# Performance work log

Hardware: AMD Instinct MI355X
Metric: run time of the kernel (lower is better)

## Reference

```python
import jax, jax.numpy as jnp
import numpy as np

NUM_HEADS = 16
LN_EPS = 1e-5

def _gelu(x):
    return jax.nn.gelu(x, approximate=False)  # torch default GELU is exact (erf)

def setup_inputs() -> dict:
    key = jax.random.key(0)
    ks = jax.random.split(key, 12)
    B, S, E = 2, 2048, 1024
    H = E // 2
    s = lambda fan_in: 1.0 / np.sqrt(fan_in)
    inp = {
        "x": jax.random.normal(ks[0], (B, S, E), jnp.float32),
        "Wq": jax.random.normal(ks[1], (E, E), jnp.float32) * s(E),
        "bq": jnp.zeros((E,), jnp.float32),
        "Wk": jax.random.normal(ks[2], (E, E), jnp.float32) * s(E),
        "bk": jnp.zeros((E,), jnp.float32),
        "Wv": jax.random.normal(ks[3], (E, E), jnp.float32) * s(E),
        "bv": jnp.zeros((E,), jnp.float32),
        "Wo": jax.random.normal(ks[4], (E, E), jnp.float32) * s(E),
        "bo": jnp.zeros((E,), jnp.float32),
        "dp_w1": jax.random.normal(ks[5], (E, H), jnp.float32) * s(E),
        "dp_b1": jnp.zeros((H,), jnp.float32),
        "ln_g": jnp.ones((H,), jnp.float32),
        "ln_b": jnp.zeros((H,), jnp.float32),
        "dp_w2": jax.random.normal(ks[6], (H, 1), jnp.float32) * s(H),
        "dp_b2": jnp.zeros((1,), jnp.float32),
        "g_w1": jax.random.normal(ks[7], (1, 16), jnp.float32),
        "g_b1": jnp.zeros((16,), jnp.float32),
        "g_w2": jax.random.normal(ks[8], (16, 1), jnp.float32) * s(16),
        "g_b2": jnp.zeros((1,), jnp.float32),
    }
    return inp


def reference(x, Wq, bq, Wk, bk, Wv, bv, Wo, bo,
              dp_w1, dp_b1, ln_g, ln_b, dp_w2, dp_b2,
              g_w1, g_b1, g_w2, g_b2):
    B, S, E = x.shape
    Hn = NUM_HEADS
    Dh = E // Hn
    scale = Dh ** -0.5

    Q = (x @ Wq + bq).reshape(B, S, Hn, Dh)
    K = (x @ Wk + bk).reshape(B, S, Hn, Dh)
    V = (x @ Wv + bv).reshape(B, S, Hn, Dh)

    # (B, H, q, k)
    logits = jnp.einsum('bqhd,bkhd->bhqk', Q, K) * scale
    causal = jnp.tril(jnp.ones((S, S), bool))
    logits = jnp.where(causal, logits, -jnp.inf)
    attn = jax.nn.softmax(logits, axis=-1)

    # drift probe: Linear -> LayerNorm -> GELU -> Linear, squeeze -> (B, S)
    h = x @ dp_w1 + dp_b1
    mu = h.mean(-1, keepdims=True)
    var = ((h - mu) ** 2).mean(-1, keepdims=True)
    h = (h - mu) / jnp.sqrt(var + LN_EPS) * ln_g + ln_b
    drift = (_gelu(h) @ dp_w2 + dp_b2)[..., 0]

    # drift_to_gate: Linear(1,16) -> GELU -> Linear(16,1) -> Tanh -> (B, S)
    g = _gelu(drift[..., None] * g_w1[0] + g_b1)
    gate = jnp.tanh(g @ g_w2 + g_b2)[..., 0]  # (B, S), indexed by key position

    gated = attn * gate[:, None, None, :]  # dropout p=0 -> identity
    out = jnp.einsum('bhqk,bkhd->bqhd', gated, V).reshape(B, S, E)
    return out @ Wo + bo
```

## Files before the change

kernel.cpp:

```cpp
#include <hip/hip_runtime.h>
#include <math.h>
#include <stdint.h>

#define B_   2
#define S_   2048
#define E_   1024
#define NH   16
#define DH   64
#define HID  512
#define NCAT 3584
#define MTOK 4096

typedef unsigned short ushort_t;
typedef short  s16x8  __attribute__((ext_vector_type(8)));
typedef unsigned short us4 __attribute__((ext_vector_type(4)));
typedef float  f32x4  __attribute__((ext_vector_type(4)));

static constexpr float LN_EPS    = 1e-5f;
static constexpr float SCALE     = 0.125f;
static constexpr float INV_SQRT2 = 0.70710678118654752440f;

__device__ __forceinline__ float gelu_exact(float v) {
    return 0.5f * v * (1.0f + erff(v * INV_SQRT2));
}

__device__ __forceinline__ ushort_t f2bf(float f) {
    unsigned int u = __float_as_uint(f);
    unsigned int r = u + 0x7fffu + ((u >> 16) & 1u);
    return (ushort_t)(r >> 16);
}
__device__ __forceinline__ float bf2f(ushort_t s) {
    return __uint_as_float(((unsigned int)s) << 16);
}

__device__ __forceinline__ void stage16(const void* g, void* ldsbase) {
#if __has_builtin(__builtin_amdgcn_global_load_lds)
    __builtin_amdgcn_global_load_lds(
        (const __attribute__((address_space(1))) void*)g,
        (__attribute__((address_space(3))) void*)ldsbase, 16, 0, 0);
#else
    ((uint4*)ldsbase)[threadIdx.x & 63] = *(const uint4*)g;
#endif
}

__device__ __forceinline__ void xcd_swizzle(int gx, int gy, int& bx, int& by) {
    const int T = gx * gy;
    const int lin = blockIdx.y * gx + blockIdx.x;
    const int work = (lin & 7) * (T >> 3) + (lin >> 3);
    bx = work % gx;
    by = work / gx;
}

__global__ __launch_bounds__(256) void split_kernel(
    const float* __restrict__ src, ushort_t* __restrict__ dh,
    ushort_t* __restrict__ dl, int n4)
{
    int i = blockIdx.x * 256 + threadIdx.x;
    if (i >= n4) return;
    float4 v = ((const float4*)src)[i];
    float vv[4] = {v.x, v.y, v.z, v.w};
    us4 h, l;
    #pragma unroll
    for (int j = 0; j < 4; ++j) {
        ushort_t hh = f2bf(vv[j]);
        h[j] = hh;
        l[j] = f2bf(vv[j] - bf2f(hh));
    }
    *(us4*)&dh[i * 4] = h;
    *(us4*)&dl[i * 4] = l;
}

__global__ __launch_bounds__(256) void transpose_split_kernel(
    const float* __restrict__ W, int N,
    ushort_t* __restrict__ th, ushort_t* __restrict__ tl)
{
    __shared__ float tile[32][33];
    const int k0 = blockIdx.x * 32, n0 = blockIdx.y * 32;
    const int t = threadIdx.x;
    const int r = t >> 3, c4 = (t & 7) * 4;

    float4 v = *(const float4*)&W[(size_t)(k0 + r) * N + n0 + c4];
    tile[r][c4 + 0] = v.x; tile[r][c4 + 1] = v.y;
    tile[r][c4 + 2] = v.z; tile[r][c4 + 3] = v.w;
    __syncthreads();

    us4 h, l;
    #pragma unroll
    for (int i = 0; i < 4; ++i) {
        float x = tile[c4 + i][r];
        ushort_t hh = f2bf(x);
        h[i] = hh;
        l[i] = f2bf(x - bf2f(hh));
    }
    *(us4*)&th[(size_t)(n0 + r) * E_ + k0 + c4] = h;
    *(us4*)&tl[(size_t)(n0 + r) * E_ + k0 + c4] = l;
}

__global__ void concat_bias_kernel(
    const float* __restrict__ bq, const float* __restrict__ bk,
    const float* __restrict__ bv, const float* __restrict__ b1,
    float* __restrict__ bcat)
{
    int i = blockIdx.x * 256 + threadIdx.x;
    if (i >= NCAT) return;
    float v;
    if      (i < 1024) v = bq[i];
    else if (i < 2048) v = bk[i - 1024];
    else if (i < 3072) v = bv[i - 2048];
    else               v = b1[i - 3072];
    bcat[i] = v;
}

struct GemmCtx {
    int lane, w, wr, wc;
};

__device__ __forceinline__ void gemm_core(
    const ushort_t* __restrict__ Ah, const ushort_t* __restrict__ Al,
    const ushort_t* __restrict__ Bh, const ushort_t* __restrict__ Bl,
    int row0, int col0, int Kd,
    ushort_t* Ahs, ushort_t* Als, ushort_t* Bhs, ushort_t* Bls,
    f32x4 (&acc)[4][4], const GemmCtx& cx)
{
    const int lr = cx.lane >> 2;
    const int lc = (cx.lane & 3) * 8;

    for (int k0 = 0; k0 < Kd; k0 += 32) {
        #pragma unroll
        for (int ii = 0; ii < 2; ++ii) {
            const int r0 = (cx.w * 2 + ii) * 16;
            const size_t ga = (size_t)(row0 + r0 + lr) * Kd + k0 + lc;
            const size_t gb = (size_t)(col0 + r0 + lr) * Kd + k0 + lc;
            stage16(Ah + ga, &Ahs[r0 * 32]);
            stage16(Al + ga, &Als[r0 * 32]);
            stage16(Bh + gb, &Bhs[r0 * 32]);
            stage16(Bl + gb, &Bls[r0 * 32]);
        }
        __syncthreads();

        const int rA = cx.wr * 64 + (cx.lane & 15);
        const int rB = cx.wc * 64 + (cx.lane & 15);
        const int kq = (cx.lane >> 4) * 8;
        s16x8 fah[4], fal[4], fbh[4], fbl[4];
        #pragma unroll
        for (int i = 0; i < 4; ++i) {
            fah[i] = *(const s16x8*)&Ahs[(rA + i * 16) * 32 + kq];
            fal[i] = *(const s16x8*)&Als[(rA + i * 16) * 32 + kq];
            fbh[i] = *(const s16x8*)&Bhs[(rB + i * 16) * 32 + kq];
            fbl[i] = *(const s16x8*)&Bls[(rB + i * 16) * 32 + kq];
        }
        __builtin_amdgcn_s_setprio(1);
        #pragma unroll
        for (int i = 0; i < 4; ++i)
            #pragma unroll
            for (int j = 0; j < 4; ++j) {
                acc[i][j] = __builtin_amdgcn_mfma_f32_16x16x32_bf16(fah[i], fbh[j], acc[i][j], 0, 0, 0);
                acc[i][j] = __builtin_amdgcn_mfma_f32_16x16x32_bf16(fah[i], fbl[j], acc[i][j], 0, 0, 0);
                acc[i][j] = __builtin_amdgcn_mfma_f32_16x16x32_bf16(fal[i], fbh[j], acc[i][j], 0, 0, 0);
            }
        __builtin_amdgcn_s_setprio(0);
        __syncthreads();
    }
}

__global__ __launch_bounds__(256) void mfma_gemm_qkvh_kernel(
    const ushort_t* __restrict__ Ah, const ushort_t* __restrict__ Al,
    const ushort_t* __restrict__ Bh, const ushort_t* __restrict__ Bl,
    const float* __restrict__ bias,
    ushort_t* __restrict__ Qh, ushort_t* __restrict__ Ql,
    ushort_t* __restrict__ Kh, ushort_t* __restrict__ Kl,
    float* __restrict__ v32, float* __restrict__ h32)
{
    __shared__ __align__(16) ushort_t Ahs[128 * 32];
    __shared__ __align__(16) ushort_t Als[128 * 32];
    __shared__ __align__(16) ushort_t Bhs[128 * 32];
    __shared__ __align__(16) ushort_t Bls[128 * 32];

    int bx, by;
    xcd_swizzle(28, 32, bx, by);
    const int row0 = by * 128, col0 = bx * 128;

    GemmCtx cx;
    cx.lane = threadIdx.x & 63;
    cx.w    = threadIdx.x >> 6;
    cx.wr   = cx.w >> 1; cx.wc = cx.w & 1;

    f32x4 acc[4][4] = {};
    gemm_core(Ah, Al, Bh, Bl, row0, col0, E_, Ahs, Als, Bhs, Bls, acc, cx);

    const int crow = row0 + cx.wr * 64 + ((cx.lane >> 4) * 4);
    const int ccol0 = col0 + cx.wc * 64 + (cx.lane & 15);

    #pragma unroll
    for (int j = 0; j < 4; ++j) {
        const int gcol = ccol0 + j * 16;
        const float bv = bias[gcol];
        #pragma unroll
        for (int i = 0; i < 4; ++i)
            #pragma unroll
            for (int r = 0; r < 4; ++r) {
                const int row = crow + i * 16 + r;
                float val = acc[i][j][r] + bv;
                if (gcol < 1024) {
                    val *= SCALE;
                    ushort_t hi = f2bf(val);
                    Qh[(size_t)row * 1024 + gcol] = hi;
                    Ql[(size_t)row * 1024 + gcol] = f2bf(val - bf2f(hi));
                } else if (gcol < 2048) {
                    ushort_t hi = f2bf(val);
                    Kh[(size_t)row * 1024 + gcol - 1024] = hi;
                    Kl[(size_t)row * 1024 + gcol - 1024] = f2bf(val - bf2f(hi));
                } else if (gcol < 3072) {
                    v32[(size_t)row * 1024 + gcol - 2048] = val;
                } else {
                    h32[(size_t)row * 512 + gcol - 3072] = val;
                }
            }
    }
}

__global__ __launch_bounds__(256) void mfma_gemm_kernel(
    const ushort_t* __restrict__ Ah, const ushort_t* __restrict__ Al,
    const ushort_t* __restrict__ Bh, const ushort_t* __restrict__ Bl,
    const float* __restrict__ bias,
    float* __restrict__ C, int N, int Kd)
{
    __shared__ __align__(16) ushort_t Ahs[128 * 32];
    __shared__ __align__(16) ushort_t Als[128 * 32];
    __shared__ __align__(16) ushort_t Bhs[128 * 32];
    __shared__ __align__(16) ushort_t Bls[128 * 32];

    int bx, by;
    xcd_swizzle(gridDim.x, gridDim.y, bx, by);
    const int row0 = by * 128, col0 = bx * 128;

    GemmCtx cx;
    cx.lane = threadIdx.x & 63;
    cx.w    = threadIdx.x >> 6;
    cx.wr   = cx.w >> 1; cx.wc = cx.w & 1;

    f32x4 acc[4][4] = {};
    gemm_core(Ah, Al, Bh, Bl, row0, col0, Kd, Ahs, Als, Bhs, Bls, acc, cx);

    const int crow = row0 + cx.wr * 64 + ((cx.lane >> 4) * 4);
    const int ccol = col0 + cx.wc * 64 + (cx.lane & 15);
    #pragma unroll
    for (int j = 0; j < 4; ++j) {
        const float bv = bias[ccol + j * 16];
        #pragma unroll
        for (int i = 0; i < 4; ++i)
            #pragma unroll
            for (int r = 0; r < 4; ++r)
                C[(size_t)(crow + i * 16 + r) * N + ccol + j * 16] = acc[i][j][r] + bv;
    }
}

__global__ __launch_bounds__(256) void ln_gate_kernel(
    const float* __restrict__ h32,
    const float* __restrict__ lng, const float* __restrict__ lnb,
    const float* __restrict__ w2,  const float* __restrict__ b2,
    const float* __restrict__ gw1, const float* __restrict__ gb1,
    const float* __restrict__ gw2, const float* __restrict__ gb2,
    float* __restrict__ gate)
{
    const int row  = blockIdx.x * 4 + (threadIdx.x >> 6);
    const int lane = threadIdx.x & 63;
    const float* h = h32 + (size_t)row * 512;

    float4 a = *(const float4*)&h[lane * 4];
    float4 b = *(const float4*)&h[256 + lane * 4];
    float va[8] = {a.x, a.y, a.z, a.w, b.x, b.y, b.z, b.w};

    float sum = 0.f, sq = 0.f;
    #pragma unroll
    for (int j = 0; j < 8; ++j) { sum += va[j]; sq += va[j] * va[j]; }
    #pragma unroll
    for (int o = 1; o < 64; o <<= 1) {
        sum += __shfl_xor(sum, o);
        sq  += __shfl_xor(sq,  o);
    }
    const float mu  = sum * (1.f / HID);
    const float inv = 1.f / sqrtf(sq * (1.f / HID) - mu * mu + LN_EPS);

    float4 g0 = *(const float4*)&lng[lane * 4];
    float4 g1 = *(const float4*)&lng[256 + lane * 4];
    float4 o0 = *(const float4*)&lnb[lane * 4];
    float4 o1 = *(const float4*)&lnb[256 + lane * 4];
    float4 w0 = *(const float4*)&w2[lane * 4];
    float4 w1 = *(const float4*)&w2[256 + lane * 4];
    float gg[8] = {g0.x, g0.y, g0.z, g0.w, g1.x, g1.y, g1.z, g1.w};
    float bb[8] = {o0.x, o0.y, o0.z, o0.w, o1.x, o1.y, o1.z, o1.w};
    float ww[8] = {w0.x, w0.y, w0.z, w0.w, w1.x, w1.y, w1.z, w1.w};

    float part = 0.f;
    #pragma unroll
    for (int j = 0; j < 8; ++j) {
        float nx = (va[j] - mu) * inv * gg[j] + bb[j];
        part += gelu_exact(nx) * ww[j];
    }
    #pragma unroll
    for (int o = 1; o < 64; o <<= 1) part += __shfl_xor(part, o);

    if (lane == 0) {
        float drift = part + b2[0];
        float gacc = gb2[0];
        #pragma unroll
        for (int i = 0; i < 16; ++i) {
            float t = fmaf(drift, gw1[i], gb1[i]);
            gacc = fmaf(gelu_exact(t), gw2[i], gacc);
        }
        gate[row] = tanhf(gacc);
    }
}

__global__ __launch_bounds__(256) void v_transpose_kernel(
    const float* __restrict__ v32, const float* __restrict__ gate,
    ushort_t* __restrict__ Vth, ushort_t* __restrict__ Vtl)
{
    __shared__ float T[64 * 68];
    const int kt = blockIdx.x, bh = blockIdx.y;
    const int b = bh >> 4, h = bh & 15;
    const int tid = threadIdx.x;

    #pragma unroll
    for (int it = 0; it < 4; ++it) {
        int idx = tid + it * 256;
        int tokr = idx >> 4, f4 = idx & 15;
        int tok = b * S_ + kt * 64 + tokr;
        float g = gate[tok];
        float4 v = *(const float4*)&v32[(size_t)tok * 1024 + h * 64 + f4 * 4];
        T[(f4 * 4 + 0) * 68 + tokr] = v.x * g;
        T[(f4 * 4 + 1) * 68 + tokr] = v.y * g;
        T[(f4 * 4 + 2) * 68 + tokr] = v.z * g;
        T[(f4 * 4 + 3) * 68 + tokr] = v.w * g;
    }
    __syncthreads();

    const int d = tid >> 2, t0 = (tid & 3) * 16;
    const size_t obase = (size_t)bh * 64 * S_ + (size_t)d * S_ + kt * 64 + t0;
    s16x8 h8[2], l8[2];
    #pragma unroll
    for (int u = 0; u < 16; ++u) {
        float f = T[d * 68 + t0 + u];
        ushort_t hh = f2bf(f);
        h8[u >> 3][u & 7] = (short)hh;
        l8[u >> 3][u & 7] = (short)f2bf(f - bf2f(hh));
    }
    *(s16x8*)&Vth[obase]     = h8[0];
    *(s16x8*)&Vth[obase + 8] = h8[1];
    *(s16x8*)&Vtl[obase]     = l8[0];
    *(s16x8*)&Vtl[obase + 8] = l8[1];
}

__global__ __launch_bounds__(256) void attn_mfma_kernel(
    const ushort_t* __restrict__ Qh, const ushort_t* __restrict__ Ql,
    const ushort_t* __restrict__ Kh, const ushort_t* __restrict__ Kl,
    const ushort_t* __restrict__ Vth, const ushort_t* __restrict__ Vtl,
    ushort_t* __restrict__ ch, ushort_t* __restrict__ cl)
{
    __shared__ __align__(16) ushort_t Qhs[64 * 72], Qls[64 * 72];
    __shared__ __align__(16) ushort_t Khs[64 * 72], Kls[64 * 72];
    __shared__ __align__(16) ushort_t Vhs[64 * 72], Vls[64 * 72];
    __shared__ __align__(16) unsigned int Ps[4 * 16 * 68];

    const int tid  = threadIdx.x;
    const int lane = tid & 63;
    const int w    = tid >> 6;
    const int g    = lane >> 4;
    const int c    = lane & 15;

    const int lin  = blockIdx.y * 32 + blockIdx.x;
    const int work = (lin & 7) * 128 + (lin >> 3);
    const int bh   = work >> 5;
    const int qt   = 31 - (work & 31);
    const int b    = bh >> 4, h = bh & 15;
    const int q0   = qt * 64;

    const size_t qkb = (size_t)b * S_ * 1024 + h * 64;
    const size_t vtb = (size_t)bh * 64 * S_;

    #pragma unroll
    for (int it = 0; it < 2; ++it) {
        int c2 = tid + it * 256;
        int row = c2 >> 3, sl = c2 & 7;
        s16x8 vh = *(const s16x8*)&Qh[qkb + (size_t)(q0 + row) * 1024 + sl * 8];
        s16x8 vl = *(const s16x8*)&Ql[qkb + (size_t)(q0 + row) * 1024 + sl * 8];
        *(s16x8*)&Qhs[row * 72 + sl * 8] = vh;
        *(s16x8*)&Qls[row * 72 + sl * 8] = vl;
    }

    f32x4 o4[4] = {};
    float m[4], l[4];
    #pragma unroll
    for (int r = 0; r < 4; ++r) { m[r] = -INFINITY; l[r] = 0.f; }

    const int pbase = w * (16 * 68);
    __syncthreads();

    s16x8 qfh[2], qfl[2];
    #pragma unroll
    for (int ks = 0; ks < 2; ++ks) {
        qfh[ks] = *(const s16x8*)&Qhs[(w * 16 + c) * 72 + ks * 32 + g * 8];
        qfl[ks] = *(const s16x8*)&Qls[(w * 16 + c) * 72 + ks * 32 + g * 8];
    }

    const int srow = tid >> 3, ssl = tid & 7;
    const int srow1 = (tid + 256) >> 3, ssl1 = (tid + 256) & 7;

    s16x8 pkh[2], pkl[2], pvh[2], pvl[2];
    {
        pkh[0] = *(const s16x8*)&Kh [qkb + (size_t)srow  * 1024 + ssl  * 8];
        pkl[0] = *(const s16x8*)&Kl [qkb + (size_t)srow  * 1024 + ssl  * 8];
        pvh[0] = *(const s16x8*)&Vth[vtb + (size_t)srow  * S_ + ssl  * 8];
        pvl[0] = *(const s16x8*)&Vtl[vtb + (size_t)srow  * S_ + ssl  * 8];
        pkh[1] = *(const s16x8*)&Kh [qkb + (size_t)srow1 * 1024 + ssl1 * 8];
        pkl[1] = *(const s16x8*)&Kl [qkb + (size_t)srow1 * 1024 + ssl1 * 8];
        pvh[1] = *(const s16x8*)&Vth[vtb + (size_t)srow1 * S_ + ssl1 * 8];
        pvl[1] = *(const s16x8*)&Vtl[vtb + (size_t)srow1 * S_ + ssl1 * 8];
    }

    for (int kt = 0; kt <= qt; ++kt) {
        const int k0 = kt * 64;
        *(s16x8*)&Khs[srow  * 72 + ssl  * 8] = pkh[0];
        *(s16x8*)&Kls[srow  * 72 + ssl  * 8] = pkl[0];
        *(s16x8*)&Vhs[srow  * 72 + ssl  * 8] = pvh[0];
        *(s16x8*)&Vls[srow  * 72 + ssl  * 8] = pvl[0];
        *(s16x8*)&Khs[srow1 * 72 + ssl1 * 8] = pkh[1];
        *(s16x8*)&Kls[srow1 * 72 + ssl1 * 8] = pkl[1];
        *(s16x8*)&Vhs[srow1 * 72 + ssl1 * 8] = pvh[1];
        *(s16x8*)&Vls[srow1 * 72 + ssl1 * 8] = pvl[1];
        __syncthreads();

        if (kt < qt) {
            const int kn = k0 + 64;
            pkh[0] = *(const s16x8*)&Kh [qkb + (size_t)(kn + srow)  * 1024 + ssl  * 8];
            pkl[0] = *(const s16x8*)&Kl [qkb + (size_t)(kn + srow)  * 1024 + ssl  * 8];
            pvh[0] = *(const s16x8*)&Vth[vtb + (size_t)srow  * S_ + kn + ssl  * 8];
            pvl[0] = *(const s16x8*)&Vtl[vtb + (size_t)srow  * S_ + kn + ssl  * 8];
            pkh[1] = *(const s16x8*)&Kh [qkb + (size_t)(kn + srow1) * 1024 + ssl1 * 8];
            pkl[1] = *(const s16x8*)&Kl [qkb + (size_t)(kn + srow1) * 1024 + ssl1 * 8];
            pvh[1] = *(const s16x8*)&Vth[vtb + (size_t)srow1 * S_ + kn + ssl1 * 8];
            pvl[1] = *(const s16x8*)&Vtl[vtb + (size_t)srow1 * S_ + kn + ssl1 * 8];
        }

        f32x4 s4[4] = {};
        __builtin_amdgcn_s_setprio(1);
        #pragma unroll
        for (int j = 0; j < 4; ++j)
            #pragma unroll
            for (int ks = 0; ks < 2; ++ks) {
                s16x8 kfh = *(const s16x8*)&Khs[(c + j * 16) * 72 + ks * 32 + g * 8];
                s16x8 kfl = *(const s16x8*)&Kls[(c + j * 16) * 72 + ks * 32 + g * 8];
                s4[j] = __builtin_amdgcn_mfma_f32_16x16x32_bf16(qfh[ks], kfh, s4[j], 0, 0, 0);
                s4[j] = __builtin_amdgcn_mfma_f32_16x16x32_bf16(qfh[ks], kfl, s4[j], 0, 0, 0);
                s4[j] = __builtin_amdgcn_mfma_f32_16x16x32_bf16(qfl[ks], kfh, s4[j], 0, 0, 0);
            }
        __builtin_amdgcn_s_setprio(0);

        if (kt == qt) {
            #pragma unroll
            for (int j = 0; j < 4; ++j)
                #pragma unroll
                for (int r = 0; r < 4; ++r)
                    if (k0 + c + j * 16 > q0 + w * 16 + g * 4 + r)
                        s4[j][r] = -INFINITY;
        }

        #pragma unroll
        for (int r = 0; r < 4; ++r) {
            float mx = fmaxf(fmaxf(s4[0][r], s4[1][r]), fmaxf(s4[2][r], s4[3][r]));
            #pragma unroll
            for (int o = 1; o < 16; o <<= 1) mx = fmaxf(mx, __shfl_xor(mx, o));
            float mn = fmaxf(m[r], mx);
            float corr = (m[r] == -INFINITY) ? 0.f : __expf(m[r] - mn);
            float ps = 0.f;
            #pragma unroll
            for (int j = 0; j < 4; ++j) {
                float p = __expf(s4[j][r] - mn);
                s4[j][r] = p;
                ps += p;
            }
            #pragma unroll
            for (int o = 1; o < 16; o <<= 1) ps += __shfl_xor(ps, o);
            l[r] = l[r] * corr + ps;
            m[r] = mn;
            #pragma unroll
            for (int j = 0; j < 4; ++j) o4[j][r] *= corr;
        }

        #pragma unroll
        for (int j = 0; j < 4; ++j)
            #pragma unroll
            for (int r = 0; r < 4; ++r) {
                float p = s4[j][r];
                ushort_t hi = f2bf(p);
                ushort_t lo = f2bf(p - bf2f(hi));
                Ps[pbase + (g * 4 + r) * 68 + c + j * 16] =
                    (unsigned int)hi | ((unsigned int)lo << 16);
            }
        asm volatile("s_waitcnt lgkmcnt(0)" ::: "memory");
        __builtin_amdgcn_sched_barrier(0);

        s16x8 pah[2], pal[2];
        #pragma unroll
        for (int ks = 0; ks < 2; ++ks) {
            uint4 a = *(const uint4*)&Ps[pbase + c * 68 + ks * 32 + g * 8];
            uint4 bq = *(const uint4*)&Ps[pbase + c * 68 + ks * 32 + g * 8 + 4];
            unsigned int wd[8] = {a.x, a.y, a.z, a.w, bq.x, bq.y, bq.z, bq.w};
            union { unsigned int u[4]; s16x8 v; } uh, ul;
            #pragma unroll
            for (int t = 0; t < 4; ++t) {
                uh.u[t] = (wd[2 * t] & 0xffffu) | (wd[2 * t + 1] << 16);
                ul.u[t] = (wd[2 * t] >> 16) | (wd[2 * t + 1] & 0xffff0000u);
            }
            pah[ks] = uh.v;
            pal[ks] = ul.v;
        }

        __builtin_amdgcn_s_setprio(1);
        #pragma unroll
        for (int j = 0; j < 4; ++j)
            #pragma unroll
            for (int ks = 0; ks < 2; ++ks) {
                s16x8 vfh = *(const s16x8*)&Vhs[(c + j * 16) * 72 + ks * 32 + g * 8];
                s16x8 vfl = *(const s16x8*)&Vls[(c + j * 16) * 72 + ks * 32 + g * 8];
                o4[j] = __builtin_amdgcn_mfma_f32_16x16x32_bf16(pah[ks], vfh, o4[j], 0, 0, 0);
                o4[j] = __builtin_amdgcn_mfma_f32_16x16x32_bf16(pah[ks], vfl, o4[j], 0, 0, 0);
                o4[j] = __builtin_amdgcn_mfma_f32_16x16x32_bf16(pal[ks], vfh, o4[j], 0, 0, 0);
            }
        __builtin_amdgcn_s_setprio(0);
        __syncthreads();
    }

    float inv[4];
    #pragma unroll
    for (int r = 0; r < 4; ++r) inv[r] = 1.f / l[r];
    #pragma unroll
    for (int j = 0; j < 4; ++j)
        #pragma unroll
        for (int r = 0; r < 4; ++r) {
            float val = o4[j][r] * inv[r];
            int tok = b * S_ + q0 + w * 16 + g * 4 + r;
            int col = h * 64 + c + j * 16;
            ushort_t hi = f2bf(val);
            ch[(size_t)tok * 1024 + col] = hi;
            cl[(size_t)tok * 1024 + col] = f2bf(val - bf2f(hi));
        }
}

extern "C" void kernel_launch(void* const* d_in, const int* in_sizes, int n_in,
                              void* d_out, int out_size, void* d_ws, size_t ws_size,
                              hipStream_t stream)
{
    const float* x    = (const float*)d_in[0];
    const float* Wq   = (const float*)d_in[1];  const float* bq   = (const float*)d_in[2];
    const float* Wk   = (const float*)d_in[3];  const float* bk   = (const float*)d_in[4];
    const float* Wv   = (const float*)d_in[5];  const float* bv   = (const float*)d_in[6];
    const float* Wo   = (const float*)d_in[7];  const float* bo   = (const float*)d_in[8];
    const float* dpw1 = (const float*)d_in[9];  const float* dpb1 = (const float*)d_in[10];
    const float* lng  = (const float*)d_in[11]; const float* lnb  = (const float*)d_in[12];
    const float* dpw2 = (const float*)d_in[13]; const float* dpb2 = (const float*)d_in[14];
    const float* gw1  = (const float*)d_in[15]; const float* gb1  = (const float*)d_in[16];
    const float* gw2  = (const float*)d_in[17]; const float* gb2  = (const float*)d_in[18];
    float* out = (float*)d_out;

    float* ws   = (float*)d_ws;
    float* v32  = ws;
    float* h32  = v32 + (size_t)MTOK * E_;
    float* bcat = h32 + (size_t)MTOK * HID;
    float* gate = bcat + NCAT;
    ushort_t* bp   = (ushort_t*)(gate + MTOK);
    ushort_t* xh   = bp;
    ushort_t* xl   = xh  + (size_t)MTOK * E_;
    ushort_t* bth  = xl  + (size_t)MTOK * E_;
    ushort_t* btl  = bth + (size_t)NCAT * E_;
    ushort_t* woth = btl + (size_t)NCAT * E_;
    ushort_t* wotl = woth + (size_t)E_ * E_;
    ushort_t* Qhb  = wotl + (size_t)E_ * E_;
    ushort_t* Qlb  = Qhb + (size_t)MTOK * E_;
    ushort_t* Khb  = Qlb + (size_t)MTOK * E_;
    ushort_t* Klb  = Khb + (size_t)MTOK * E_;
    ushort_t* Vthb = Klb + (size_t)MTOK * E_;
    ushort_t* Vtlb = Vthb + (size_t)MTOK * E_;
    ushort_t* chb  = xh;
    ushort_t* clb  = xl;

    hipLaunchKernelGGL(split_kernel, dim3(4096), dim3(256), 0, stream,
                       x, xh, xl, MTOK * E_ / 4);
    hipLaunchKernelGGL(transpose_split_kernel, dim3(32, 32), dim3(256), 0, stream,
                       Wq, E_, bth, btl);
    hipLaunchKernelGGL(transpose_split_kernel, dim3(32, 32), dim3(256), 0, stream,
                       Wk, E_, bth + (size_t)1024 * E_, btl + (size_t)1024 * E_);
    hipLaunchKernelGGL(transpose_split_kernel, dim3(32, 32), dim3(256), 0, stream,
                       Wv, E_, bth + (size_t)2048 * E_, btl + (size_t)2048 * E_);
    hipLaunchKernelGGL(transpose_split_kernel, dim3(32, 16), dim3(256), 0, stream,
                       dpw1, HID, bth + (size_t)3072 * E_, btl + (size_t)3072 * E_);
    hipLaunchKernelGGL(transpose_split_kernel, dim3(32, 32), dim3(256), 0, stream,
                       Wo, E_, woth, wotl);
    hipLaunchKernelGGL(concat_bias_kernel, dim3(14), dim3(256), 0, stream,
                       bq, bk, bv, dpb1, bcat);

    hipLaunchKernelGGL(mfma_gemm_qkvh_kernel, dim3(28, 32), dim3(256), 0, stream,
                       xh, xl, bth, btl, bcat, Qhb, Qlb, Khb, Klb, v32, h32);

    hipLaunchKernelGGL(ln_gate_kernel, dim3(MTOK / 4), dim3(256), 0, stream,
                       h32, lng, lnb, dpw2, dpb2, gw1, gb1, gw2, gb2, gate);
    hipLaunchKernelGGL(v_transpose_kernel, dim3(32, 32), dim3(256), 0, stream,
                       v32, gate, Vthb, Vtlb);

    hipLaunchKernelGGL(attn_mfma_kernel, dim3(S_ / 64, B_ * NH), dim3(256), 0, stream,
                       Qhb, Qlb, Khb, Klb, Vthb, Vtlb, chb, clb);

    hipLaunchKernelGGL(mfma_gemm_kernel, dim3(E_ / 128, MTOK / 128), dim3(256), 0, stream,
                       chb, clb, woth, wotl, bo, out, E_, E_);
}
```

Baseline: 440.3 us.

## Widen attention query tile to 128 rows with 8 waves sharing K/V tiles

The attention kernel now processes 128 query rows per block with 512 threads (8 waves), so each staged 64-key K/V tile feeds twice as many query rows and global K/V traffic per query is halved. Shared memory is packed into one buffer, with the P scratch area aliasing the Q staging area, which is dead once Q fragments are in registers. Waves whose 16 rows lie entirely before a key tile skip that tile's MFMA and softmax work. The costs are fewer blocks in the grid, larger causal imbalance inside a block, and a tighter register budget from the launch bounds.

```diff
diff --git a/kernel.cpp b/kernel.cpp
--- a/kernel.cpp
+++ b/kernel.cpp
@@ -352,16 +352,20 @@
     *(s16x8*)&Vtl[obase + 8] = l8[1];
 }
 
-__global__ __launch_bounds__(256) void attn_mfma_kernel(
+__global__ __launch_bounds__(512, 4) void attn_mfma_kernel(
     const ushort_t* __restrict__ Qh, const ushort_t* __restrict__ Ql,
     const ushort_t* __restrict__ Kh, const ushort_t* __restrict__ Kl,
     const ushort_t* __restrict__ Vth, const ushort_t* __restrict__ Vtl,
     ushort_t* __restrict__ ch, ushort_t* __restrict__ cl)
 {
-    __shared__ __align__(16) ushort_t Qhs[64 * 72], Qls[64 * 72];
-    __shared__ __align__(16) ushort_t Khs[64 * 72], Kls[64 * 72];
-    __shared__ __align__(16) ushort_t Vhs[64 * 72], Vls[64 * 72];
-    __shared__ __align__(16) unsigned int Ps[4 * 16 * 68];
+    __shared__ __align__(16) ushort_t smem[36864];
+    ushort_t* const Qhs = smem;
+    ushort_t* const Qls = smem + 9216;
+    ushort_t* const Khs = smem + 18432;
+    ushort_t* const Kls = smem + 23040;
+    ushort_t* const Vhs = smem + 27648;
+    ushort_t* const Vls = smem + 32256;
+    unsigned int* const Ps = (unsigned int*)smem;
 
     const int tid  = threadIdx.x;
     const int lane = tid & 63;
@@ -369,19 +373,19 @@
     const int g    = lane >> 4;
     const int c    = lane & 15;
 
-    const int lin  = blockIdx.y * 32 + blockIdx.x;
-    const int work = (lin & 7) * 128 + (lin >> 3);
-    const int bh   = work >> 5;
-    const int qt   = 31 - (work & 31);
+    const int lin  = blockIdx.y * 16 + blockIdx.x;
+    const int work = (lin & 7) * 64 + (lin >> 3);
+    const int bh   = work >> 4;
+    const int qt   = 15 - (work & 15);
     const int b    = bh >> 4, h = bh & 15;
-    const int q0   = qt * 64;
+    const int q0   = qt * 128;
 
     const size_t qkb = (size_t)b * S_ * 1024 + h * 64;
     const size_t vtb = (size_t)bh * 64 * S_;
 
     #pragma unroll
     for (int it = 0; it < 2; ++it) {
-        int c2 = tid + it * 256;
+        int c2 = tid + it * 512;
         int row = c2 >> 3, sl = c2 & 7;
         s16x8 vh = *(const s16x8*)&Qh[qkb + (size_t)(q0 + row) * 1024 + sl * 8];
         s16x8 vl = *(const s16x8*)&Ql[qkb + (size_t)(q0 + row) * 1024 + sl * 8];
@@ -405,130 +409,120 @@
     }
 
     const int srow = tid >> 3, ssl = tid & 7;
-    const int srow1 = (tid + 256) >> 3, ssl1 = (tid + 256) & 7;
-
-    s16x8 pkh[2], pkl[2], pvh[2], pvl[2];
-    {
-        pkh[0] = *(const s16x8*)&Kh [qkb + (size_t)srow  * 1024 + ssl  * 8];
-        pkl[0] = *(const s16x8*)&Kl [qkb + (size_t)srow  * 1024 + ssl  * 8];
-        pvh[0] = *(const s16x8*)&Vth[vtb + (size_t)srow  * S_ + ssl  * 8];
-        pvl[0] = *(const s16x8*)&Vtl[vtb + (size_t)srow  * S_ + ssl  * 8];
-        pkh[1] = *(const s16x8*)&Kh [qkb + (size_t)srow1 * 1024 + ssl1 * 8];
-        pkl[1] = *(const s16x8*)&Kl [qkb + (size_t)srow1 * 1024 + ssl1 * 8];
-        pvh[1] = *(const s16x8*)&Vth[vtb + (size_t)srow1 * S_ + ssl1 * 8];
-        pvl[1] = *(const s16x8*)&Vtl[vtb + (size_t)srow1 * S_ + ssl1 * 8];
-    }
-
-    for (int kt = 0; kt <= qt; ++kt) {
+
+    s16x8 pkh, pkl, pvh, pvl;
+    pkh = *(const s16x8*)&Kh [qkb + (size_t)srow * 1024 + ssl * 8];
+    pkl = *(const s16x8*)&Kl [qkb + (size_t)srow * 1024 + ssl * 8];
+    pvh = *(const s16x8*)&Vth[vtb + (size_t)srow * S_ + ssl * 8];
+    pvl = *(const s16x8*)&Vtl[vtb + (size_t)srow * S_ + ssl * 8];
+
+    const int ktmax = 2 * qt + 1;
+    const int qwave = q0 + w * 16;
+
+    for (int kt = 0; kt <= ktmax; ++kt) {
         const int k0 = kt * 64;
-        *(s16x8*)&Khs[srow  * 72 + ssl  * 8] = pkh[0];
-        *(s16x8*)&Kls[srow  * 72 + ssl  * 8] = pkl[0];
-        *(s16x8*)&Vhs[srow  * 72 + ssl  * 8] = pvh[0];
-        *(s16x8*)&Vls[srow  * 72 + ssl  * 8] = pvl[0];
-        *(s16x8*)&Khs[srow1 * 72 + ssl1 * 8] = pkh[1];
-        *(s16x8*)&Kls[srow1 * 72 + ssl1 * 8] = pkl[1];
-        *(s16x8*)&Vhs[srow1 * 72 + ssl1 * 8] = pvh[1];
-        *(s16x8*)&Vls[srow1 * 72 + ssl1 * 8] = pvl[1];
+        *(s16x8*)&Khs[srow * 72 + ssl * 8] = pkh;
+        *(s16x8*)&Kls[srow * 72 + ssl * 8] = pkl;
+        *(s16x8*)&Vhs[srow * 72 + ssl * 8] = pvh;
+        *(s16x8*)&Vls[srow * 72 + ssl * 8] = pvl;
         __syncthreads();
 
-        if (kt < qt) {
+        if (kt < ktmax) {
             const int kn = k0 + 64;
-            pkh[0] = *(const s16x8*)&Kh [qkb + (size_t)(kn + srow)  * 1024 + ssl  * 8];
-            pkl[0] = *(const s16x8*)&Kl [qkb + (size_t)(kn + srow)  * 1024 + ssl  * 8];
-            pvh[0] = *(const s16x8*)&Vth[vtb + (size_t)srow  * S_ + kn + ssl  * 8];
-            pvl[0] = *(const s16x8*)&Vtl[vtb + (size_t)srow  * S_ + kn + ssl  * 8];
-            pkh[1] = *(const s16x8*)&Kh [qkb + (size_t)(kn + srow1) * 1024 + ssl1 * 8];
-            pkl[1] = *(const s16x8*)&Kl [qkb + (size_t)(kn + srow1) * 1024 + ssl1 * 8];
-            pvh[1] = *(const s16x8*)&Vth[vtb + (size_t)srow1 * S_ + kn + ssl1 * 8];
-            pvl[1] = *(const s16x8*)&Vtl[vtb + (size_t)srow1 * S_ + kn + ssl1 * 8];
+            pkh = *(const s16x8*)&Kh [qkb + (size_t)(kn + srow) * 1024 + ssl * 8];
+            pkl = *(const s16x8*)&Kl [qkb + (size_t)(kn + srow) * 1024 + ssl * 8];
+            pvh = *(const s16x8*)&Vth[vtb + (size_t)srow * S_ + kn + ssl * 8];
+            pvl = *(const s16x8*)&Vtl[vtb + (size_t)srow * S_ + kn + ssl * 8];
         }
 
-        f32x4 s4[4] = {};
-        __builtin_amdgcn_s_setprio(1);
-        #pragma unroll
-        for (int j = 0; j < 4; ++j)
+        if (k0 <= qwave + 15) {
+            f32x4 s4[4] = {};
+            __builtin_amdgcn_s_setprio(1);
+            #pragma unroll
+            for (int j = 0; j < 4; ++j)
+                #pragma unroll
+                for (int ks = 0; ks < 2; ++ks) {
+                    s16x8 kfh = *(const s16x8*)&Khs[(c + j * 16) * 72 + ks * 32 + g * 8];
+                    s16x8 kfl = *(const s16x8*)&Kls[(c + j * 16) * 72 + ks * 32 + g * 8];
+                    s4[j] = __builtin_amdgcn_mfma_f32_16x16x32_bf16(qfh[ks], kfh, s4[j], 0, 0, 0);
+                    s4[j] = __builtin_amdgcn_mfma_f32_16x16x32_bf16(qfh[ks], kfl, s4[j], 0, 0, 0);
+                    s4[j] = __builtin_amdgcn_mfma_f32_16x16x32_bf16(qfl[ks], kfh, s4[j], 0, 0, 0);
+                }
+            __builtin_amdgcn_s_setprio(0);
+
+            if (k0 + 63 > qwave) {
+                #pragma unroll
+                for (int j = 0; j < 4; ++j)
+                    #pragma unroll
+                    for (int r = 0; r < 4; ++r)
+                        if (k0 + c + j * 16 > qwave + g * 4 + r)
+                            s4[j][r] = -INFINITY;
+            }
+
+            #pragma unroll
+            for (int r = 0; r < 4; ++r) {
+                float mx = fmaxf(fmaxf(s4[0][r], s4[1][r]), fmaxf(s4[2][r], s4[3][r]));
+                #pragma unroll
+                for (int o = 1; o < 16; o <<= 1) mx = fmaxf(mx, __shfl_xor(mx, o));
+                float mn = fmaxf(m[r], mx);
+                float corr = (m[r] == -INFINITY) ? 0.f : __expf(m[r] - mn);
+                float ps = 0.f;
+                #pragma unroll
+                for (int j = 0; j < 4; ++j) {
+                    float p = __expf(s4[j][r] - mn);
+                    s4[j][r] = p;
+                    ps += p;
+                }
+                #pragma unroll
+                for (int o = 1; o < 16; o <<= 1) ps += __shfl_xor(ps, o);
+                l[r] = l[r] * corr + ps;
+                m[r] = mn;
+                #pragma unroll
+                for (int j = 0; j < 4; ++j) o4[j][r] *= corr;
+            }
+
+            #pragma unroll
+            for (int j = 0; j < 4; ++j)
+                #pragma unroll
+                for (int r = 0; r < 4; ++r) {
+                    float p = s4[j][r];
+                    ushort_t hi = f2bf(p);
+                    ushort_t lo = f2bf(p - bf2f(hi));
+                    Ps[pbase + (g * 4 + r) * 68 + c + j * 16] =
+                        (unsigned int)hi | ((unsigned int)lo << 16);
+                }
+            asm volatile("s_waitcnt lgkmcnt(0)" ::: "memory");
+            __builtin_amdgcn_sched_barrier(0);
+
+            s16x8 pah[2], pal[2];
             #pragma unroll
             for (int ks = 0; ks < 2; ++ks) {
-                s16x8 kfh = *(const s16x8*)&Khs[(c + j * 16) * 72 + ks * 32 + g * 8];
-                s16x8 kfl = *(const s16x8*)&Kls[(c + j * 16) * 72 + ks * 32 + g * 8];
-                s4[j] = __builtin_amdgcn_mfma_f32_16x16x32_bf16(qfh[ks], kfh, s4[j], 0, 0, 0);
-                s4[j] = __builtin_amdgcn_mfma_f32_16x16x32_bf16(qfh[ks], kfl, s4[j], 0, 0, 0);
-                s4[j] = __builtin_amdgcn_mfma_f32_16x16x32_bf16(qfl[ks], kfh, s4[j], 0, 0, 0);
+                uint4 a = *(const uint4*)&Ps[pbase + c * 68 + ks * 32 + g * 8];
+                uint4 bq = *(const uint4*)&Ps[pbase + c * 68 + ks * 32 + g * 8 + 4];
+                unsigned int wd[8] = {a.x, a.y, a.z, a.w, bq.x, bq.y, bq.z, bq.w};
+                union { unsigned int u[4]; s16x8 v; } uh, ul;
+                #pragma unroll
+                for (int t = 0; t < 4; ++t) {
+                    uh.u[t] = (wd[2 * t] & 0xffffu) | (wd[2 * t + 1] << 16);
+                    ul.u[t] = (wd[2 * t] >> 16) | (wd[2 * t + 1] & 0xffff0000u);
+                }
+                pah[ks] = uh.v;
+                pal[ks] = ul.v;
             }
-        __builtin_amdgcn_s_setprio(0);
-
-        if (kt == qt) {
+
+            __builtin_amdgcn_s_setprio(1);
             #pragma unroll
             for (int j = 0; j < 4; ++j)
                 #pragma unroll
-                for (int r = 0; r < 4; ++r)
-                    if (k0 + c + j * 16 > q0 + w * 16 + g * 4 + r)
-                        s4[j][r] = -INFINITY;
+                for (int ks = 0; ks < 2; ++ks) {
+                    s16x8 vfh = *(const s16x8*)&Vhs[(c + j * 16) * 72 + ks * 32 + g * 8];
+                    s16x8 vfl = *(const s16x8*)&Vls[(c + j * 16) * 72 + ks * 32 + g * 8];
+                    o4[j] = __builtin_amdgcn_mfma_f32_16x16x32_bf16(pah[ks], vfh, o4[j], 0, 0, 0);
+                    o4[j] = __builtin_amdgcn_mfma_f32_16x16x32_bf16(pah[ks], vfl, o4[j], 0, 0, 0);
+                    o4[j] = __builtin_amdgcn_mfma_f32_16x16x32_bf16(pal[ks], vfh, o4[j], 0, 0, 0);
+                }
+            __builtin_amdgcn_s_setprio(0);
         }
-
-        #pragma unroll
-        for (int r = 0; r < 4; ++r) {
-            float mx = fmaxf(fmaxf(s4[0][r], s4[1][r]), fmaxf(s4[2][r], s4[3][r]));
-            #pragma unroll
-            for (int o = 1; o < 16; o <<= 1) mx = fmaxf(mx, __shfl_xor(mx, o));
-            float mn = fmaxf(m[r], mx);
-            float corr = (m[r] == -INFINITY) ? 0.f : __expf(m[r] - mn);
-            float ps = 0.f;
-            #pragma unroll
-            for (int j = 0; j < 4; ++j) {
-                float p = __expf(s4[j][r] - mn);
-                s4[j][r] = p;
-                ps += p;
-            }
-            #pragma unroll
-            for (int o = 1; o < 16; o <<= 1) ps += __shfl_xor(ps, o);
-            l[r] = l[r] * corr + ps;
-            m[r] = mn;
-            #pragma unroll
-            for (int j = 0; j < 4; ++j) o4[j][r] *= corr;
-        }
-
-        #pragma unroll
-        for (int j = 0; j < 4; ++j)
-            #pragma unroll
-            for (int r = 0; r < 4; ++r) {
-                float p = s4[j][r];
-                ushort_t hi = f2bf(p);
-                ushort_t lo = f2bf(p - bf2f(hi));
-                Ps[pbase + (g * 4 + r) * 68 + c + j * 16] =
-                    (unsigned int)hi | ((unsigned int)lo << 16);
-            }
-        asm volatile("s_waitcnt lgkmcnt(0)" ::: "memory");
-        __builtin_amdgcn_sched_barrier(0);
-
-        s16x8 pah[2], pal[2];
-        #pragma unroll
-        for (int ks = 0; ks < 2; ++ks) {
-            uint4 a = *(const uint4*)&Ps[pbase + c * 68 + ks * 32 + g * 8];
-            uint4 bq = *(const uint4*)&Ps[pbase + c * 68 + ks * 32 + g * 8 + 4];
-            unsigned int wd[8] = {a.x, a.y, a.z, a.w, bq.x, bq.y, bq.z, bq.w};
-            union { unsigned int u[4]; s16x8 v; } uh, ul;
-            #pragma unroll
-            for (int t = 0; t < 4; ++t) {
-                uh.u[t] = (wd[2 * t] & 0xffffu) | (wd[2 * t + 1] << 16);
-                ul.u[t] = (wd[2 * t] >> 16) | (wd[2 * t + 1] & 0xffff0000u);
-            }
-            pah[ks] = uh.v;
-            pal[ks] = ul.v;
-        }
-
-        __builtin_amdgcn_s_setprio(1);
-        #pragma unroll
-        for (int j = 0; j < 4; ++j)
-            #pragma unroll
-            for (int ks = 0; ks < 2; ++ks) {
-                s16x8 vfh = *(const s16x8*)&Vhs[(c + j * 16) * 72 + ks * 32 + g * 8];
-                s16x8 vfl = *(const s16x8*)&Vls[(c + j * 16) * 72 + ks * 32 + g * 8];
-                o4[j] = __builtin_amdgcn_mfma_f32_16x16x32_bf16(pah[ks], vfh, o4[j], 0, 0, 0);
-                o4[j] = __builtin_amdgcn_mfma_f32_16x16x32_bf16(pah[ks], vfl, o4[j], 0, 0, 0);
-                o4[j] = __builtin_amdgcn_mfma_f32_16x16x32_bf16(pal[ks], vfh, o4[j], 0, 0, 0);
-            }
-        __builtin_amdgcn_s_setprio(0);
         __syncthreads();
     }
 
@@ -608,7 +602,7 @@
     hipLaunchKernelGGL(v_transpose_kernel, dim3(32, 32), dim3(256), 0, stream,
                        v32, gate, Vthb, Vtlb);
 
-    hipLaunchKernelGGL(attn_mfma_kernel, dim3(S_ / 64, B_ * NH), dim3(256), 0, stream,
+    hipLaunchKernelGGL(attn_mfma_kernel, dim3(S_ / 128, B_ * NH), dim3(512), 0, stream,
                        Qhb, Qlb, Khb, Klb, Vthb, Vtlb, chb, clb);
 
     hipLaunchKernelGGL(mfma_gemm_kernel, dim3(E_ / 128, MTOK / 128), dim3(256), 0, stream,
```

Result: no change. 447.2 us (+1.6%).
